# Optimization experiments

Hardware: AMD Instinct MI355X
Metric: run time of the kernel (lower is better)

The kernel has to match this reference:

```python
import jax, jax.numpy as jnp
import numpy as np

T, B, H, L = 1024, 256, 120, 4  # time, batch, hidden, layers


def setup_inputs() -> dict:
    key = jax.random.key(0)
    ks = jax.random.split(key, 10)
    s = 1.0 / np.sqrt(H)  # PyTorch LSTM init scale
    u = lambda k, shape: jax.random.uniform(k, shape, jnp.float32, -s, s)
    return {
        "x": jax.random.normal(ks[0], (T, B), jnp.float32),
        "h0": jax.random.uniform(ks[1], (L, B, H), jnp.float32),
        "c0": jax.random.uniform(ks[2], (L, B, H), jnp.float32),
        "W_ih0": u(ks[3], (4 * H, 1)),
        "W_ih": u(ks[4], (L - 1, 4 * H, H)),
        "W_hh": u(ks[5], (L, 4 * H, H)),
        "b_ih": u(ks[6], (L, 4 * H)),
        "b_hh": u(ks[7], (L, 4 * H)),
        "W_lin": u(ks[8], (1, H)),
        "b_lin": u(ks[9], (1,)),
    }


def _lstm_cell(x, h, c, gates_x):
    # gates_x: precomputed x @ W_ih^T + b_ih part already folded by caller
    raise NotImplementedError  # unused helper placeholder


def reference(x, h0, c0, W_ih0, W_ih, W_hh, b_ih, b_hh, W_lin, b_lin):
    def step(carry, x_t):
        h, c = carry                      # each [L, B, H]
        inp = x_t[:, None]                # [B, 1]
        new_h, new_c = [], []
        for l in range(L):
            Wih = W_ih0 if l == 0 else W_ih[l - 1]
            gates = inp @ Wih.T + b_ih[l] + h[l] @ W_hh[l].T + b_hh[l]  # [B, 4H]
            i_g, f_g, g_g, o_g = jnp.split(gates, 4, axis=-1)  # PyTorch gate order i,f,g,o
            c_l = jax.nn.sigmoid(f_g) * c[l] + jax.nn.sigmoid(i_g) * jnp.tanh(g_g)
            h_l = jax.nn.sigmoid(o_g) * jnp.tanh(c_l)
            new_h.append(h_l)
            new_c.append(c_l)
            inp = h_l
        out_t = (inp @ W_lin.T + b_lin)[:, 0]  # [B]
        return (jnp.stack(new_h), jnp.stack(new_c)), out_t

    _, outputs = jax.lax.scan(step, (h0, c0), x)  # outputs: [T, B]
    return outputs
```

## Files before the change

kernel.cpp:

```cpp
#include <hip/hip_runtime.h>
#include <hip/hip_fp16.h>
#include <math.h>

#define Tn 1024
#define Bn 256
#define Hn 120
#define Ln 4
#define NBC 16
#define NBCOL 16
#define NBLK (Ln*NBC)
#define THR 512
#define Dd 16
#define PADI 32
#define KPh 520
#define ENT 2048

typedef _Float16 f16x8 __attribute__((ext_vector_type(8)));
typedef float    f32x4 __attribute__((ext_vector_type(4)));
typedef unsigned int u32x2 __attribute__((ext_vector_type(2)));
typedef unsigned short ushort_t;

template<int N> struct IC { static constexpr int value = N; };

__device__ ushort_t g_ring[(size_t)3 * Dd * NBC * ENT];
__device__ int g_prod[3 * NBC * PADI];
__device__ int g_cons[Ln * NBC * PADI];
__device__ int g_abort;

__global__ __launch_bounds__(256) void init_kernel() {
    int idx = threadIdx.x;
    if (idx < 3 * NBC)  g_prod[idx * PADI] = -1;
    if (idx < Ln * NBC) g_cons[idx * PADI] = -1;
    if (idx == 0)       g_abort = 0;
}

#if __has_builtin(__builtin_amdgcn_exp2f)
__device__ __forceinline__ float hw_exp2(float x) { return __builtin_amdgcn_exp2f(x); }
#else
__device__ __forceinline__ float hw_exp2(float x) { return exp2f(x); }
#endif
#if __has_builtin(__builtin_amdgcn_rcpf)
__device__ __forceinline__ float hw_rcp(float x) { return __builtin_amdgcn_rcpf(x); }
#else
__device__ __forceinline__ float hw_rcp(float x) { return 1.0f / x; }
#endif
#define LOG2E_F 1.44269504f

__device__ __forceinline__ float sigm(float v) {
    return hw_rcp(1.0f + hw_exp2(-LOG2E_F * v));
}
__device__ __forceinline__ float tanh_fast(float v) {
    return 1.0f - 2.0f * hw_rcp(1.0f + hw_exp2(2.0f * LOG2E_F * v));
}

#define BAR_LGKM() asm volatile("s_waitcnt lgkmcnt(0)\ns_barrier" ::: "memory")

__device__ __forceinline__ void spin_wait(int* p, int tgt, int& dead, int& pc) {
    if (dead || pc >= tgt) return;
    int guard = 0, v;
    while ((v = __hip_atomic_load(p, __ATOMIC_RELAXED,
                                  __HIP_MEMORY_SCOPE_SYSTEM)) < tgt) {
        __builtin_amdgcn_s_sleep(1);
        if ((++guard & 127) == 0) {
            if (__hip_atomic_load(&g_abort, __ATOMIC_RELAXED,
                                  __HIP_MEMORY_SCOPE_SYSTEM)) { dead = 1; return; }
            if (guard > 60000) { atomicExch(&g_abort, 1); dead = 1; return; }
        }
    }
    pc = v;
}

__device__ __forceinline__ void post_flag(int* p, int v) {
    __hip_atomic_store(p, v, __ATOMIC_RELAXED, __HIP_MEMORY_SCOPE_SYSTEM);
}

__global__ __launch_bounds__(THR, 2) void lstm_kernel(
    const float* __restrict__ x,    const float* __restrict__ h0,
    const float* __restrict__ c0,   const float* __restrict__ Wih0,
    const float* __restrict__ Wih,  const float* __restrict__ Whh,
    const float* __restrict__ bih,  const float* __restrict__ bhh,
    const float* __restrict__ Wlin, const float* __restrict__ blin,
    float* __restrict__ out)
{
    __shared__ _Float16 hxT[NBCOL * KPh];

    const int bx   = blockIdx.x;
    const int l    = bx >> 4;
    const int bc   = bx & 15;
    const int tid  = threadIdx.x;
    const int w    = tid >> 6;
    const int lane = tid & 63;
    const int quad = lane >> 4;
    const int l16  = lane & 15;
    const int bg0  = bc * NBCOL;
    const int mtn  = (w < 6) ? 4 : 3;
    const int mt0  = (w < 6) ? 4 * w : 24 + 3 * (w - 6);
    int dead = 0, pcb = -0x40000000, pca = -0x40000000;

    const float* WhhL = Whh + (size_t)l * 4 * Hn * Hn;
    const float* WihL = (l > 0) ? Wih + (size_t)(l - 1) * 4 * Hn * Hn : Whh;
    ushort_t* ringP = g_ring + (size_t)l * Dd * NBC * ENT;
    const ushort_t* ringC =
        g_ring + (size_t)(l > 0 ? l - 1 : 0) * Dd * NBC * ENT;
    int* prodUp = &g_prod[(l > 0 ? ((l - 1) * NBC + bc) : 0) * PADI];
    int* prodMe = &g_prod[(l < 3 ? (l * NBC + bc) : 0) * PADI];
    int* consDn = &g_cons[(l < 3 ? ((l + 1) * NBC + bc) : 0) * PADI];
    int* consMe = &g_cons[(l * NBC + bc) * PADI];

    f16x8 a[4][8];
    #pragma unroll
    for (int m = 0; m < 4; ++m) {
        int rp = (mt0 + m) * 16 + l16;
        int cell = rp >> 2, gate = rp & 3;
        int orow = gate * Hn + cell;
        #pragma unroll
        for (int kt = 0; kt < 8; ++kt) {
            f16x8 av;
            #pragma unroll
            for (int j = 0; j < 8; ++j) {
                int k = kt * 32 + quad * 8 + j;
                float v = 0.f;
                if (m < mtn) {
                    if (k < Hn)          v = WhhL[orow * Hn + k];
                    else if (l == 0)     { if (k == 120) v = Wih0[orow]; }
                    else if (k >= 128) {
                        int s = k - 128, w2 = s >> 4, r = s & 15;
                        int q2 = r >> 2, m2 = r & 3;
                        int mtn2 = (w2 < 6) ? 4 : 3;
                        int mt02 = (w2 < 6) ? 4 * w2 : 24 + 3 * (w2 - 6);
                        if (m2 < mtn2)
                            v = WihL[orow * Hn + (mt02 + m2) * 4 + q2];
                    }
                }
                av[j] = (_Float16)v;
            }
            a[m][kt] = av;
        }
    }

    float bias_g[4][4];
    float cst[4];
    #pragma unroll
    for (int m = 0; m < 4; ++m) {
        int cell = (mt0 + m) * 4 + quad;
        #pragma unroll
        for (int g = 0; g < 4; ++g)
            bias_g[m][g] = (m < mtn)
                ? bih[l * 4 * Hn + g * Hn + cell] + bhh[l * 4 * Hn + g * Hn + cell]
                : 0.f;
        cst[m] = (m < mtn) ? c0[(l * Bn + bg0 + l16) * Hn + cell] : 0.f;
    }

    const int sg_col = (tid >> 2) & 15;
    const int sg_w   = tid >> 6;
    const int sg_q   = tid & 3;
    const int sg_lds = sg_col * KPh + 128 + sg_w * 16 + sg_q * 4;

    const int oc_col = tid >> 3, oc_j = tid & 7;
    float wl[15];
    if (l == 3) {
        #pragma unroll
        for (int c2 = 0; c2 < 15; ++c2) wl[c2] = Wlin[oc_j * 15 + c2];
    }

    for (int q2 = tid; q2 < NBCOL * KPh; q2 += THR) hxT[q2] = (_Float16)0.f;
    __syncthreads();
    for (int q2 = tid; q2 < NBCOL * Hn; q2 += THR) {
        int col = q2 / Hn, cell = q2 % Hn;
        hxT[col * KPh + 256 + cell] = (_Float16)h0[(l * Bn + bg0 + col) * Hn + cell];
    }
    __syncthreads();

    if (l > 0) {
        spin_wait(prodUp, 0, dead, pcb);
        u32x2 v0 = {0, 0};
        const ushort_t* p = ringC + (size_t)(0 * NBC + bc) * ENT + tid * 4;
        asm volatile("global_load_dwordx2 %0, %1, off sc0 sc1"
                     : "=v"(v0) : "v"(p));
        asm volatile("s_waitcnt vmcnt(0)" ::: "memory");
        *(u32x2*)&hxT[sg_lds] = v0;
        __syncthreads();
        if (tid == 96) post_flag(consMe, 0);
    } else {
        if (tid < NBCOL) hxT[tid * KPh + 256 + 120] = (_Float16)x[bg0 + tid];
        __syncthreads();
    }

    auto run = [&](auto ktlc) {
        constexpr int KTL = decltype(ktlc)::value;
        for (int t = 0; t < Tn; ++t) {
            const int slotW = t & (Dd - 1);
            const int slotR = (t + 1) & (Dd - 1);
            const int q  = t & 1;
            const int hR = (q ^ 1) << 8;
            const int hW = q << 8;

            if ((t & 3) == 0) {
                if (l > 0) {
                    int tgt = (t + 4 < Tn) ? t + 4 : Tn - 1;
                    spin_wait(prodUp, tgt, dead, pcb);
                }
                if (l < 3 && t >= 16)
                    spin_wait(consDn, t - 13, dead, pca);
            }

            u32x2 ld = {0, 0};
            float xr = 0.f;
            if (l > 0 && (t + 1) < Tn) {
                const ushort_t* p = ringC + (size_t)(slotR * NBC + bc) * ENT + tid * 4;
                asm volatile("global_load_dwordx2 %0, %1, off sc0 sc1"
                             : "=v"(ld) : "v"(p));
            }
            if (l == 0 && (t + 1) < Tn && tid < NBCOL)
                xr = x[(t + 1) * Bn + bg0 + tid];

            f32x4 acc[4];
            #pragma unroll
            for (int m = 0; m < 4; ++m) {
                f32x4 z; z[0] = bias_g[m][0]; z[1] = bias_g[m][1];
                z[2] = bias_g[m][2]; z[3] = bias_g[m][3];
                acc[m] = z;
            }
            unsigned short hb[4] = {0, 0, 0, 0};

            #pragma unroll
            for (int half = 0; half < 2; ++half) {
                const int M0 = half * 2;
                #pragma unroll
                for (int kt = 0; kt < KTL; ++kt) {
                    const int e0 = kt * 32 + quad * 8;
                    const int ao = e0 + ((kt < 4) ? hR : (q << 8));
                    f16x8 bfr = *(const f16x8*)&hxT[l16 * KPh + ao];
                    #pragma unroll
                    for (int m = M0; m < M0 + 2; ++m)
                        if (m < mtn)
                            acc[m] = __builtin_amdgcn_mfma_f32_16x16x32_f16(
                                a[m][kt], bfr, acc[m], 0, 0, 0);
                }
                #pragma unroll
                for (int m = M0; m < M0 + 2; ++m) {
                    if (m >= mtn) continue;
                    int cell = (mt0 + m) * 4 + quad;
                    float ig = sigm(acc[m][0]);
                    float fg = sigm(acc[m][1]);
                    float gg = tanh_fast(acc[m][2]);
                    float og = sigm(acc[m][3]);
                    float cn = fmaf(fg, cst[m], ig * gg);
                    cst[m] = cn;
                    float hn = og * tanh_fast(cn);
                    _Float16 hh = (_Float16)hn;
                    hxT[l16 * KPh + hW + cell] = hh;
                    hb[m] = __builtin_bit_cast(unsigned short, hh);
                }
            }

            if (l < 3) {
                u32x2 sv;
                sv[0] = (unsigned)hb[0] | ((unsigned)hb[1] << 16);
                sv[1] = (unsigned)hb[2] | ((unsigned)hb[3] << 16);
                ushort_t* p0 = ringP + (size_t)(slotW * NBC + bc) * ENT
                             + w * 256 + l16 * 16 + quad * 4;
                asm volatile("global_store_dwordx2 %0, %1, off sc0 sc1"
                             :: "v"(p0), "v"(sv) : "memory");
            }

            if (l < 3) { asm volatile("s_waitcnt vmcnt(1)" ::: "memory"); }
            else       { asm volatile("s_waitcnt vmcnt(0)" ::: "memory"); }
            __builtin_amdgcn_sched_barrier(0);

            if (l > 0 && (t + 1) < Tn)
                *(u32x2*)&hxT[sg_lds + ((q ^ 1) << 8)] = ld;
            if (l == 0 && (t + 1) < Tn && tid < NBCOL)
                hxT[tid * KPh + hW + 120] = (_Float16)xr;

            BAR_LGKM();

            if (l == 3 && tid < NBCOL * 8) {
                float pout = 0.f;
                const _Float16* hrow = &hxT[oc_col * KPh + hW + oc_j * 15];
                #pragma unroll
                for (int c2 = 0; c2 < 15; ++c2)
                    pout = fmaf(wl[c2], (float)hrow[c2], pout);
                pout += __shfl_down(pout, 4, 8);
                pout += __shfl_down(pout, 2, 8);
                pout += __shfl_down(pout, 1, 8);
                if (oc_j == 0) out[t * Bn + bg0 + oc_col] = pout + blin[0];
            }

            if ((t & 3) == 3) {
                if (l < 3 && tid == 0)  post_flag(prodMe, t - 1);
                if (l > 0 && tid == 96) post_flag(consMe, t + 1);
            }
        }
    };
    if (l == 0) run(IC<4>{});
    else        run(IC<8>{});

    if (l < 3) {
        asm volatile("s_waitcnt vmcnt(0)" ::: "memory");
        __syncthreads();
        if (tid == 0) post_flag(prodMe, Tn - 1);
    }
}

extern "C" void kernel_launch(void* const* d_in, const int* in_sizes, int n_in,
                              void* d_out, int out_size, void* d_ws, size_t ws_size,
                              hipStream_t stream) {
    const float* x    = (const float*)d_in[0];
    const float* h0   = (const float*)d_in[1];
    const float* c0   = (const float*)d_in[2];
    const float* Wih0 = (const float*)d_in[3];
    const float* Wih  = (const float*)d_in[4];
    const float* Whh  = (const float*)d_in[5];
    const float* bih  = (const float*)d_in[6];
    const float* bhh  = (const float*)d_in[7];
    const float* Wlin = (const float*)d_in[8];
    const float* blin = (const float*)d_in[9];
    float* out = (float*)d_out;

    hipLaunchKernelGGL(init_kernel, dim3(1), dim3(256), 0, stream);
    hipLaunchKernelGGL(lstm_kernel, dim3(NBLK), dim3(THR), 0, stream,
                       x, h0, c0, Wih0, Wih, Whh, bih, bhh, Wlin, blin, out);
}
```

Measured before the change: 1.532 ms.

## Prefetch ring inputs two timesteps ahead with unrolled double-buffered step loop

Unrolls the timestep loop by two with compile-time parity, so LDS offsets become constants. Ring loads for the next layer's input (and x for layer 0) are now issued two steps ahead into alternating register buffers, and the waitcnt is relaxed to vmcnt(2). The consumer flag and the producer wait targets shift by one step to match the deeper prefetch. All threads now compute the output dot product with masked column indices instead of branching on tid. This gives more latency hiding for cross-block ring loads, at the cost of tighter slack in the producer/consumer ring protocol and redundant work in the output stage.

New measurement: 1.948 ms. 27.1% more time.

```diff
diff --git a/kernel.cpp b/kernel.cpp
--- a/kernel.cpp
+++ b/kernel.cpp
@@ -156,7 +156,7 @@
     const int sg_q   = tid & 3;
     const int sg_lds = sg_col * KPh + 128 + sg_w * 16 + sg_q * 4;
 
-    const int oc_col = tid >> 3, oc_j = tid & 7;
+    const int oc_col = (tid >> 3) & 15, oc_j = tid & 7;
     float wl[15];
     if (l == 3) {
         #pragma unroll
@@ -171,48 +171,58 @@
     }
     __syncthreads();
 
+    u32x2 ldA = {0, 0}, ldB = {0, 0};
+    float xrA = 0.f, xrB = 0.f;
     if (l > 0) {
-        spin_wait(prodUp, 0, dead, pcb);
+        spin_wait(prodUp, 1, dead, pcb);
         u32x2 v0 = {0, 0};
-        const ushort_t* p = ringC + (size_t)(0 * NBC + bc) * ENT + tid * 4;
+        const ushort_t* p0 = ringC + (size_t)(0 * NBC + bc) * ENT + tid * 4;
+        const ushort_t* p1 = ringC + (size_t)(1 * NBC + bc) * ENT + tid * 4;
         asm volatile("global_load_dwordx2 %0, %1, off sc0 sc1"
-                     : "=v"(v0) : "v"(p));
+                     : "=v"(v0) : "v"(p0));
+        asm volatile("global_load_dwordx2 %0, %1, off sc0 sc1"
+                     : "=v"(ldB) : "v"(p1));
         asm volatile("s_waitcnt vmcnt(0)" ::: "memory");
+        __builtin_amdgcn_sched_barrier(0);
         *(u32x2*)&hxT[sg_lds] = v0;
         __syncthreads();
-        if (tid == 96) post_flag(consMe, 0);
+        if (tid == 96) post_flag(consMe, 1);
     } else {
         if (tid < NBCOL) hxT[tid * KPh + 256 + 120] = (_Float16)x[bg0 + tid];
+        xrB = x[Bn + bg0 + (tid & 15)];
         __syncthreads();
     }
 
     auto run = [&](auto ktlc) {
         constexpr int KTL = decltype(ktlc)::value;
-        for (int t = 0; t < Tn; ++t) {
+
+        auto step = [&](int t, auto par, u32x2& ld_i, u32x2& ld_s,
+                        float& xr_i, float& xr_s) {
+            constexpr int P  = decltype(par)::value;
+            constexpr int hR = (P ^ 1) << 8;
+            constexpr int hW = P << 8;
             const int slotW = t & (Dd - 1);
-            const int slotR = (t + 1) & (Dd - 1);
-            const int q  = t & 1;
-            const int hR = (q ^ 1) << 8;
-            const int hW = q << 8;
+            const int slotL = (t + 2) & (Dd - 1);
 
             if ((t & 3) == 0) {
                 if (l > 0) {
-                    int tgt = (t + 4 < Tn) ? t + 4 : Tn - 1;
+                    int tgt = (t + 5 < Tn) ? t + 5 : Tn - 1;
                     spin_wait(prodUp, tgt, dead, pcb);
                 }
                 if (l < 3 && t >= 16)
                     spin_wait(consDn, t - 13, dead, pca);
             }
 
-            u32x2 ld = {0, 0};
-            float xr = 0.f;
-            if (l > 0 && (t + 1) < Tn) {
-                const ushort_t* p = ringC + (size_t)(slotR * NBC + bc) * ENT + tid * 4;
+            if (l > 0 && (t + 2) < Tn) {
+                const ushort_t* p = ringC + (size_t)(slotL * NBC + bc) * ENT + tid * 4;
                 asm volatile("global_load_dwordx2 %0, %1, off sc0 sc1"
-                             : "=v"(ld) : "v"(p));
-            }
-            if (l == 0 && (t + 1) < Tn && tid < NBCOL)
-                xr = x[(t + 1) * Bn + bg0 + tid];
+                             : "=v"(ld_i) : "v"(p));
+            }
+            if (l == 0 && (t + 2) < Tn) {
+                const float* px = x + (size_t)(t + 2) * Bn + bg0 + (tid & 15);
+                asm volatile("global_load_dword %0, %1, off"
+                             : "=v"(xr_i) : "v"(px));
+            }
 
             f32x4 acc[4];
             #pragma unroll
@@ -229,7 +239,7 @@
                 #pragma unroll
                 for (int kt = 0; kt < KTL; ++kt) {
                     const int e0 = kt * 32 + quad * 8;
-                    const int ao = e0 + ((kt < 4) ? hR : (q << 8));
+                    const int ao = e0 + ((kt < 4) ? hR : hW);
                     f16x8 bfr = *(const f16x8*)&hxT[l16 * KPh + ao];
                     #pragma unroll
                     for (int m = M0; m < M0 + 2; ++m)
@@ -264,18 +274,17 @@
                              :: "v"(p0), "v"(sv) : "memory");
             }
 
-            if (l < 3) { asm volatile("s_waitcnt vmcnt(1)" ::: "memory"); }
-            else       { asm volatile("s_waitcnt vmcnt(0)" ::: "memory"); }
+            asm volatile("s_waitcnt vmcnt(2)" ::: "memory");
             __builtin_amdgcn_sched_barrier(0);
 
             if (l > 0 && (t + 1) < Tn)
-                *(u32x2*)&hxT[sg_lds + ((q ^ 1) << 8)] = ld;
-            if (l == 0 && (t + 1) < Tn && tid < NBCOL)
-                hxT[tid * KPh + hW + 120] = (_Float16)xr;
+                *(u32x2*)&hxT[sg_lds + ((P ^ 1) << 8)] = ld_s;
+            if (l == 0 && (t + 1) < Tn && tid < 16)
+                hxT[tid * KPh + hW + 120] = (_Float16)xr_s;
 
             BAR_LGKM();
 
-            if (l == 3 && tid < NBCOL * 8) {
+            if (l == 3) {
                 float pout = 0.f;
                 const _Float16* hrow = &hxT[oc_col * KPh + hW + oc_j * 15];
                 #pragma unroll
@@ -288,9 +297,14 @@
             }
 
             if ((t & 3) == 3) {
-                if (l < 3 && tid == 0)  post_flag(prodMe, t - 1);
+                if (l < 3 && tid == 0)  post_flag(prodMe, t - 2);
                 if (l > 0 && tid == 96) post_flag(consMe, t + 1);
             }
+        };
+
+        for (int t = 0; t < Tn; t += 2) {
+            step(t,     IC<0>{}, ldA, ldB, xrA, xrB);
+            step(t + 1, IC<1>{}, ldB, ldA, xrB, xrA);
         }
     };
     if (l == 0) run(IC<4>{});
```

## Add dedicated producer-consumer wavefront for ring loads and flag synchronization

Applied to the files above, without the earlier changes.

Adds a ninth wavefront per block that handles all inter-layer ring-buffer loads, x prefetch, spin-waits and consumer flag posting. The eight compute wavefronts now only do the MFMA gate math and publish their outputs. The loader prefetches two steps ahead with double-buffered registers, which should take global latency and spin waits off the compute critical path. The cost is a larger block, launch bounds relaxed to one block per CU, and a single wave issuing all loads. It also adds more intricate barrier matching between the two roles, which risks deadlock.

After: 3.065 ms. 100.0% more time.

```diff
diff --git a/kernel.cpp b/kernel.cpp
--- a/kernel.cpp
+++ b/kernel.cpp
@@ -9,7 +9,7 @@
 #define NBC 16
 #define NBCOL 16
 #define NBLK (Ln*NBC)
-#define THR 512
+#define THR 576
 #define Dd 16
 #define PADI 32
 #define KPh 520
@@ -74,7 +74,7 @@
     __hip_atomic_store(p, v, __ATOMIC_RELAXED, __HIP_MEMORY_SCOPE_SYSTEM);
 }
 
-__global__ __launch_bounds__(THR, 2) void lstm_kernel(
+__global__ __launch_bounds__(THR, 1) void lstm_kernel(
     const float* __restrict__ x,    const float* __restrict__ h0,
     const float* __restrict__ c0,   const float* __restrict__ Wih0,
     const float* __restrict__ Wih,  const float* __restrict__ Whh,
@@ -93,9 +93,6 @@
     const int quad = lane >> 4;
     const int l16  = lane & 15;
     const int bg0  = bc * NBCOL;
-    const int mtn  = (w < 6) ? 4 : 3;
-    const int mt0  = (w < 6) ? 4 * w : 24 + 3 * (w - 6);
-    int dead = 0, pcb = -0x40000000, pca = -0x40000000;
 
     const float* WhhL = Whh + (size_t)l * 4 * Hn * Hn;
     const float* WihL = (l > 0) ? Wih + (size_t)(l - 1) * 4 * Hn * Hn : Whh;
@@ -107,194 +104,245 @@
     int* consDn = &g_cons[(l < 3 ? ((l + 1) * NBC + bc) : 0) * PADI];
     int* consMe = &g_cons[(l * NBC + bc) * PADI];
 
-    f16x8 a[4][8];
-    #pragma unroll
-    for (int m = 0; m < 4; ++m) {
-        int rp = (mt0 + m) * 16 + l16;
-        int cell = rp >> 2, gate = rp & 3;
-        int orow = gate * Hn + cell;
-        #pragma unroll
-        for (int kt = 0; kt < 8; ++kt) {
-            f16x8 av;
-            #pragma unroll
-            for (int j = 0; j < 8; ++j) {
-                int k = kt * 32 + quad * 8 + j;
-                float v = 0.f;
-                if (m < mtn) {
-                    if (k < Hn)          v = WhhL[orow * Hn + k];
-                    else if (l == 0)     { if (k == 120) v = Wih0[orow]; }
-                    else if (k >= 128) {
-                        int s = k - 128, w2 = s >> 4, r = s & 15;
-                        int q2 = r >> 2, m2 = r & 3;
-                        int mtn2 = (w2 < 6) ? 4 : 3;
-                        int mt02 = (w2 < 6) ? 4 * w2 : 24 + 3 * (w2 - 6);
-                        if (m2 < mtn2)
-                            v = WihL[orow * Hn + (mt02 + m2) * 4 + q2];
-                    }
-                }
-                av[j] = (_Float16)v;
-            }
-            a[m][kt] = av;
-        }
-    }
-
-    float bias_g[4][4];
-    float cst[4];
-    #pragma unroll
-    for (int m = 0; m < 4; ++m) {
-        int cell = (mt0 + m) * 4 + quad;
-        #pragma unroll
-        for (int g = 0; g < 4; ++g)
-            bias_g[m][g] = (m < mtn)
-                ? bih[l * 4 * Hn + g * Hn + cell] + bhh[l * 4 * Hn + g * Hn + cell]
-                : 0.f;
-        cst[m] = (m < mtn) ? c0[(l * Bn + bg0 + l16) * Hn + cell] : 0.f;
-    }
-
-    const int sg_col = (tid >> 2) & 15;
-    const int sg_w   = tid >> 6;
-    const int sg_q   = tid & 3;
-    const int sg_lds = sg_col * KPh + 128 + sg_w * 16 + sg_q * 4;
-
-    const int oc_col = tid >> 3, oc_j = tid & 7;
-    float wl[15];
-    if (l == 3) {
-        #pragma unroll
-        for (int c2 = 0; c2 < 15; ++c2) wl[c2] = Wlin[oc_j * 15 + c2];
-    }
-
     for (int q2 = tid; q2 < NBCOL * KPh; q2 += THR) hxT[q2] = (_Float16)0.f;
     __syncthreads();
     for (int q2 = tid; q2 < NBCOL * Hn; q2 += THR) {
         int col = q2 / Hn, cell = q2 % Hn;
         hxT[col * KPh + 256 + cell] = (_Float16)h0[(l * Bn + bg0 + col) * Hn + cell];
     }
+    if (l == 0 && tid < NBCOL)
+        hxT[tid * KPh + 256 + 120] = (_Float16)x[bg0 + tid];
     __syncthreads();
 
-    if (l > 0) {
-        spin_wait(prodUp, 0, dead, pcb);
-        u32x2 v0 = {0, 0};
-        const ushort_t* p = ringC + (size_t)(0 * NBC + bc) * ENT + tid * 4;
-        asm volatile("global_load_dwordx2 %0, %1, off sc0 sc1"
-                     : "=v"(v0) : "v"(p));
-        asm volatile("s_waitcnt vmcnt(0)" ::: "memory");
-        *(u32x2*)&hxT[sg_lds] = v0;
-        __syncthreads();
-        if (tid == 96) post_flag(consMe, 0);
+    if (w < 8) {
+        const int mtn = (w < 6) ? 4 : 3;
+        const int mt0 = (w < 6) ? 4 * w : 24 + 3 * (w - 6);
+
+        f16x8 a[4][8];
+        #pragma unroll
+        for (int m = 0; m < 4; ++m) {
+            int rp = (mt0 + m) * 16 + l16;
+            int cell = rp >> 2, gate = rp & 3;
+            int orow = gate * Hn + cell;
+            #pragma unroll
+            for (int kt = 0; kt < 8; ++kt) {
+                f16x8 av;
+                #pragma unroll
+                for (int j = 0; j < 8; ++j) {
+                    int k = kt * 32 + quad * 8 + j;
+                    float v = 0.f;
+                    if (m < mtn) {
+                        if (k < Hn)          v = WhhL[orow * Hn + k];
+                        else if (l == 0)     { if (k == 120) v = Wih0[orow]; }
+                        else if (k >= 128) {
+                            int s = k - 128, w2 = s >> 4, r = s & 15;
+                            int q2 = r >> 2, m2 = r & 3;
+                            int mtn2 = (w2 < 6) ? 4 : 3;
+                            int mt02 = (w2 < 6) ? 4 * w2 : 24 + 3 * (w2 - 6);
+                            if (m2 < mtn2)
+                                v = WihL[orow * Hn + (mt02 + m2) * 4 + q2];
+                        }
+                    }
+                    av[j] = (_Float16)v;
+                }
+                a[m][kt] = av;
+            }
+        }
+
+        float bias_g[4][4];
+        float cst[4];
+        #pragma unroll
+        for (int m = 0; m < 4; ++m) {
+            int cell = (mt0 + m) * 4 + quad;
+            #pragma unroll
+            for (int g = 0; g < 4; ++g)
+                bias_g[m][g] = (m < mtn)
+                    ? bih[l * 4 * Hn + g * Hn + cell] + bhh[l * 4 * Hn + g * Hn + cell]
+                    : 0.f;
+            cst[m] = (m < mtn) ? c0[(l * Bn + bg0 + l16) * Hn + cell] : 0.f;
+        }
+
+        const int oc_col = tid >> 3, oc_j = tid & 7;
+        float wl[15];
+        if (l == 3) {
+            #pragma unroll
+            for (int c2 = 0; c2 < 15; ++c2) wl[c2] = Wlin[oc_j * 15 + c2];
+        }
+
+        if (l > 0) __syncthreads();
+
+        auto run = [&](auto ktlc) {
+            constexpr int KTL = decltype(ktlc)::value;
+            for (int t = 0; t < Tn; ++t) {
+                const int q  = t & 1;
+                const int hR = (q ^ 1) << 8;
+                const int hW = q << 8;
+
+                f32x4 acc[4];
+                #pragma unroll
+                for (int m = 0; m < 4; ++m) {
+                    f32x4 z; z[0] = bias_g[m][0]; z[1] = bias_g[m][1];
+                    z[2] = bias_g[m][2]; z[3] = bias_g[m][3];
+                    acc[m] = z;
+                }
+                unsigned short hb[4] = {0, 0, 0, 0};
+
+                #pragma unroll
+                for (int half = 0; half < 2; ++half) {
+                    const int M0 = half * 2;
+                    #pragma unroll
+                    for (int kt = 0; kt < KTL; ++kt) {
+                        const int e0 = kt * 32 + quad * 8;
+                        const int ao = e0 + ((kt < 4) ? hR : (q << 8));
+                        f16x8 bfr = *(const f16x8*)&hxT[l16 * KPh + ao];
+                        #pragma unroll
+                        for (int m = M0; m < M0 + 2; ++m)
+                            if (m < mtn)
+                                acc[m] = __builtin_amdgcn_mfma_f32_16x16x32_f16(
+                                    a[m][kt], bfr, acc[m], 0, 0, 0);
+                    }
+                    #pragma unroll
+                    for (int m = M0; m < M0 + 2; ++m) {
+                        if (m >= mtn) continue;
+                        int cell = (mt0 + m) * 4 + quad;
+                        float ig = sigm(acc[m][0]);
+                        float fg = sigm(acc[m][1]);
+                        float gg = tanh_fast(acc[m][2]);
+                        float og = sigm(acc[m][3]);
+                        float cn = fmaf(fg, cst[m], ig * gg);
+                        cst[m] = cn;
+                        float hn = og * tanh_fast(cn);
+                        _Float16 hh = (_Float16)hn;
+                        hxT[l16 * KPh + hW + cell] = hh;
+                        hb[m] = __builtin_bit_cast(unsigned short, hh);
+                    }
+                }
+
+                if (l < 3) {
+                    u32x2 sv;
+                    sv[0] = (unsigned)hb[0] | ((unsigned)hb[1] << 16);
+                    sv[1] = (unsigned)hb[2] | ((unsigned)hb[3] << 16);
+                    ushort_t* p0 = ringP + (size_t)((t & (Dd - 1)) * NBC + bc) * ENT
+                                 + w * 256 + l16 * 16 + quad * 4;
+                    asm volatile("global_store_dwordx2 %0, %1, off sc0 sc1"
+                                 :: "v"(p0), "v"(sv) : "memory");
+                    asm volatile("s_waitcnt vmcnt(1)" ::: "memory");
+                }
+
+                BAR_LGKM();
+
+                if (l == 3 && tid < NBCOL * 8) {
+                    float pout = 0.f;
+                    const _Float16* hrow = &hxT[oc_col * KPh + hW + oc_j * 15];
+                    #pragma unroll
+                    for (int c2 = 0; c2 < 15; ++c2)
+                        pout = fmaf(wl[c2], (float)hrow[c2], pout);
+                    pout += __shfl_down(pout, 4, 8);
+                    pout += __shfl_down(pout, 2, 8);
+                    pout += __shfl_down(pout, 1, 8);
+                    if (oc_j == 0) out[t * Bn + bg0 + oc_col] = pout + blin[0];
+                }
+                if ((t & 3) == 3 && l < 3 && tid == 0)
+                    post_flag(prodMe, t - 1);
+            }
+        };
+        if (l == 0) run(IC<4>{});
+        else        run(IC<8>{});
     } else {
-        if (tid < NBCOL) hxT[tid * KPh + 256 + 120] = (_Float16)x[bg0 + tid];
-        __syncthreads();
-    }
-
-    auto run = [&](auto ktlc) {
-        constexpr int KTL = decltype(ktlc)::value;
-        for (int t = 0; t < Tn; ++t) {
-            const int slotW = t & (Dd - 1);
-            const int slotR = (t + 1) & (Dd - 1);
-            const int q  = t & 1;
-            const int hR = (q ^ 1) << 8;
-            const int hW = q << 8;
-
+        int dead = 0, pcb = -0x40000000, pca = -0x40000000;
+        int sgo[8];
+        #pragma unroll
+        for (int i = 0; i < 8; ++i) {
+            int v = i * 64 + lane;
+            int col = (v >> 2) & 15, w2 = v >> 6, q2 = v & 3;
+            sgo[i] = col * KPh + 128 + w2 * 16 + q2 * 4;
+        }
+        u32x2 ldA[8], ldB[8];
+        #pragma unroll
+        for (int i = 0; i < 8; ++i) { ldA[i] = (u32x2){0,0}; ldB[i] = (u32x2){0,0}; }
+        float xrA = 0.f, xrB = 0.f;
+
+        if (l > 0) {
+            spin_wait(prodUp, 1, dead, pcb);
+            const ushort_t* b0 = ringC + (size_t)(0 * NBC + bc) * ENT;
+            const ushort_t* b1 = ringC + (size_t)(1 * NBC + bc) * ENT;
+            u32x2 v0[8];
+            #pragma unroll
+            for (int i = 0; i < 8; ++i) {
+                const ushort_t* p = b0 + (i * 64 + lane) * 4;
+                asm volatile("global_load_dwordx2 %0, %1, off sc0 sc1"
+                             : "=v"(v0[i]) : "v"(p));
+            }
+            #pragma unroll
+            for (int i = 0; i < 8; ++i) {
+                const ushort_t* p = b1 + (i * 64 + lane) * 4;
+                asm volatile("global_load_dwordx2 %0, %1, off sc0 sc1"
+                             : "=v"(ldA[i]) : "v"(p));
+            }
+            asm volatile("s_waitcnt vmcnt(0)" ::: "memory");
+            __builtin_amdgcn_sched_barrier(0);
+            #pragma unroll
+            for (int i = 0; i < 8; ++i)
+                *(u32x2*)&hxT[sgo[i]] = v0[i];
+            __syncthreads();
+            if (lane == 0) post_flag(consMe, 1);
+        } else {
+            if (lane < NBCOL) xrA = x[Bn + bg0 + lane];
+        }
+
+        auto dstep = [&](int t, auto par, u32x2 (&ldS)[8], u32x2 (&ldI)[8],
+                         float& xrS, float& xrI) {
+            constexpr int P = decltype(par)::value;
             if ((t & 3) == 0) {
                 if (l > 0) {
-                    int tgt = (t + 4 < Tn) ? t + 4 : Tn - 1;
+                    int tgt = (t + 5 < Tn) ? t + 5 : Tn - 1;
                     spin_wait(prodUp, tgt, dead, pcb);
                 }
-                if (l < 3 && t >= 16)
-                    spin_wait(consDn, t - 13, dead, pca);
-            }
-
-            u32x2 ld = {0, 0};
-            float xr = 0.f;
+                if (l < 3 && t >= 12)
+                    spin_wait(consDn, t - 12, dead, pca);
+            }
+            if (l > 0 && (t + 2) < Tn) {
+                const ushort_t* base =
+                    ringC + (size_t)(((t + 2) & (Dd - 1)) * NBC + bc) * ENT;
+                #pragma unroll
+                for (int i = 0; i < 8; ++i) {
+                    const ushort_t* p = base + (i * 64 + lane) * 4;
+                    asm volatile("global_load_dwordx2 %0, %1, off sc0 sc1"
+                                 : "=v"(ldI[i]) : "v"(p));
+                }
+            }
+            if (l == 0 && (t + 2) < Tn && lane < NBCOL) {
+                const float* px = x + (size_t)(t + 2) * Bn + bg0 + lane;
+                asm volatile("global_load_dword %0, %1, off"
+                             : "=v"(xrI) : "v"(px));
+            }
+            if (l > 0) {
+                if ((t + 2) < Tn) asm volatile("s_waitcnt vmcnt(8)" ::: "memory");
+                else              asm volatile("s_waitcnt vmcnt(0)" ::: "memory");
+            } else {
+                if ((t + 2) < Tn) asm volatile("s_waitcnt vmcnt(1)" ::: "memory");
+                else              asm volatile("s_waitcnt vmcnt(0)" ::: "memory");
+            }
+            __builtin_amdgcn_sched_barrier(0);
             if (l > 0 && (t + 1) < Tn) {
-                const ushort_t* p = ringC + (size_t)(slotR * NBC + bc) * ENT + tid * 4;
-                asm volatile("global_load_dwordx2 %0, %1, off sc0 sc1"
-                             : "=v"(ld) : "v"(p));
-            }
-            if (l == 0 && (t + 1) < Tn && tid < NBCOL)
-                xr = x[(t + 1) * Bn + bg0 + tid];
-
-            f32x4 acc[4];
-            #pragma unroll
-            for (int m = 0; m < 4; ++m) {
-                f32x4 z; z[0] = bias_g[m][0]; z[1] = bias_g[m][1];
-                z[2] = bias_g[m][2]; z[3] = bias_g[m][3];
-                acc[m] = z;
-            }
-            unsigned short hb[4] = {0, 0, 0, 0};
-
-            #pragma unroll
-            for (int half = 0; half < 2; ++half) {
-                const int M0 = half * 2;
-                #pragma unroll
-                for (int kt = 0; kt < KTL; ++kt) {
-                    const int e0 = kt * 32 + quad * 8;
-                    const int ao = e0 + ((kt < 4) ? hR : (q << 8));
-                    f16x8 bfr = *(const f16x8*)&hxT[l16 * KPh + ao];
-                    #pragma unroll
-                    for (int m = M0; m < M0 + 2; ++m)
-                        if (m < mtn)
-                            acc[m] = __builtin_amdgcn_mfma_f32_16x16x32_f16(
-                                a[m][kt], bfr, acc[m], 0, 0, 0);
-                }
-                #pragma unroll
-                for (int m = M0; m < M0 + 2; ++m) {
-                    if (m >= mtn) continue;
-                    int cell = (mt0 + m) * 4 + quad;
-                    float ig = sigm(acc[m][0]);
-                    float fg = sigm(acc[m][1]);
-                    float gg = tanh_fast(acc[m][2]);
-                    float og = sigm(acc[m][3]);
-                    float cn = fmaf(fg, cst[m], ig * gg);
-                    cst[m] = cn;
-                    float hn = og * tanh_fast(cn);
-                    _Float16 hh = (_Float16)hn;
-                    hxT[l16 * KPh + hW + cell] = hh;
-                    hb[m] = __builtin_bit_cast(unsigned short, hh);
-                }
-            }
-
-            if (l < 3) {
-                u32x2 sv;
-                sv[0] = (unsigned)hb[0] | ((unsigned)hb[1] << 16);
-                sv[1] = (unsigned)hb[2] | ((unsigned)hb[3] << 16);
-                ushort_t* p0 = ringP + (size_t)(slotW * NBC + bc) * ENT
-                             + w * 256 + l16 * 16 + quad * 4;
-                asm volatile("global_store_dwordx2 %0, %1, off sc0 sc1"
-                             :: "v"(p0), "v"(sv) : "memory");
-            }
-
-            if (l < 3) { asm volatile("s_waitcnt vmcnt(1)" ::: "memory"); }
-            else       { asm volatile("s_waitcnt vmcnt(0)" ::: "memory"); }
-            __builtin_amdgcn_sched_barrier(0);
-
-            if (l > 0 && (t + 1) < Tn)
-                *(u32x2*)&hxT[sg_lds + ((q ^ 1) << 8)] = ld;
-            if (l == 0 && (t + 1) < Tn && tid < NBCOL)
-                hxT[tid * KPh + hW + 120] = (_Float16)xr;
+                #pragma unroll
+                for (int i = 0; i < 8; ++i)
+                    *(u32x2*)&hxT[sgo[i] + ((P ^ 1) << 8)] = ldS[i];
+            }
+            if (l == 0 && (t + 1) < Tn && lane < NBCOL)
+                hxT[lane * KPh + (P << 8) + 120] = (_Float16)xrS;
 
             BAR_LGKM();
 
-            if (l == 3 && tid < NBCOL * 8) {
-                float pout = 0.f;
-                const _Float16* hrow = &hxT[oc_col * KPh + hW + oc_j * 15];
-                #pragma unroll
-                for (int c2 = 0; c2 < 15; ++c2)
-                    pout = fmaf(wl[c2], (float)hrow[c2], pout);
-                pout += __shfl_down(pout, 4, 8);
-                pout += __shfl_down(pout, 2, 8);
-                pout += __shfl_down(pout, 1, 8);
-                if (oc_j == 0) out[t * Bn + bg0 + oc_col] = pout + blin[0];
-            }
-
-            if ((t & 3) == 3) {
-                if (l < 3 && tid == 0)  post_flag(prodMe, t - 1);
-                if (l > 0 && tid == 96) post_flag(consMe, t + 1);
-            }
-        }
-    };
-    if (l == 0) run(IC<4>{});
-    else        run(IC<8>{});
+            if ((t & 3) == 3 && l > 0 && lane == 0)
+                post_flag(consMe, t + 1);
+        };
+
+        for (int t = 0; t < Tn; t += 2) {
+            dstep(t,     IC<0>{}, ldA, ldB, xrA, xrB);
+            dstep(t + 1, IC<1>{}, ldB, ldA, xrB, xrA);
+        }
+    }
 
     if (l < 3) {
         asm volatile("s_waitcnt vmcnt(0)" ::: "memory");
```
